# Kernel optimization log

Hardware: AMD Instinct MI355X
Metric: run time of the kernel (lower is better)

Reference implementation:

```python
import jax, jax.numpy as jnp
import numpy as np

N = 131072  # time steps
D = 4       # SDE state dimension


def setup_inputs() -> dict:
    key = jax.random.key(0)
    k = jax.random.split(key, 6)
    F = 0.1 * jax.random.normal(k[0], (D, D), jnp.float32)  # only shape/dtype used by filter
    H = jnp.zeros((1, D), jnp.float32).at[0, 0].set(1.0)    # observe first state component
    P_inf = jnp.eye(D, dtype=jnp.float32)
    # stable per-step transitions: spectral radius ~0.9
    A_seq = 0.9 * jnp.eye(D, dtype=jnp.float32)[None] + 0.02 * jax.random.normal(k[1], (N, D, D), jnp.float32)
    # PSD process noise per step
    S = 0.05 * jax.random.normal(k[2], (N, D, D), jnp.float32)
    Q_seq = jnp.einsum('nij,nkj->nik', S, S) + 1e-3 * jnp.eye(D, dtype=jnp.float32)[None]
    residual = jax.random.normal(k[3], (N,), jnp.float32)   # y - mean_fn(times)
    mask = jnp.ones((N,), jnp.float32)                      # all steps observed
    R_seq = 0.1 + 0.05 * jax.random.uniform(k[4], (N,), jnp.float32)  # noise_var + floor
    return dict(F=F, H=H, P_inf=P_inf, A_seq=A_seq, Q_seq=Q_seq,
                residual=residual, mask=mask, R_seq=R_seq)


def _kalman_filter(F, H, P_inf, A_seq, Q_seq, residual, mask, R_seq):
    d = F.shape[0]
    eye = jnp.eye(d, dtype=F.dtype)
    h = H[0]  # (d,)
    log_2pi = jnp.log(2.0 * jnp.pi).astype(F.dtype)

    def step(carry, inputs):
        m, P = carry
        A, Q, r_n, mask_n, R_n = inputs
        m_pred = A @ m
        P_pred = A @ P @ A.T + Q
        P_pred = 0.5 * (P_pred + P_pred.T)
        Ph = P_pred @ h                 # (d,)
        S = h @ Ph + R_n                # innovation variance
        innov = r_n - h @ m_pred
        is_obs = mask_n == 1
        S_safe = jnp.where(is_obs, S, 1.0)
        K = jnp.where(is_obs, Ph / S_safe, jnp.zeros_like(Ph))
        m_new = m_pred + K * innov
        I_KH = eye - K[:, None] * h[None, :]
        P_new = I_KH @ P_pred @ I_KH.T + R_n * (K[:, None] * K[None, :])
        P_new = 0.5 * (P_new + P_new.T)
        ll = jnp.where(is_obs, -0.5 * (log_2pi + jnp.log(S_safe) + innov * innov / S_safe), 0.0)
        return (m_new, P_new), (m_pred, P_pred, m_new, P_new, ll)

    m0 = jnp.zeros(d, dtype=F.dtype)
    _, (m_pred_seq, P_pred_seq, m_filt_seq, P_filt_seq, ll_seq) = jax.lax.scan(
        step, (m0, P_inf), (A_seq, Q_seq, residual, mask, R_seq))
    return m_pred_seq, P_pred_seq, m_filt_seq, P_filt_seq, jnp.sum(ll_seq)


def _rts_smoother(m_pred_seq, P_pred_seq, m_filt_seq, P_filt_seq, A_seq):
    def step(carry, inputs):
        m_ns, P_ns = carry
        m_f, P_f, m_pn, P_pn, A_n = inputs
        J = jnp.linalg.solve(P_pn.T, A_n @ P_f.T).T
        m_s = m_f + J @ (m_ns - m_pn)
        P_s = P_f + J @ (P_ns - P_pn) @ J.T
        P_s = 0.5 * (P_s + P_s.T)
        return (m_s, P_s), (m_s, P_s)

    m_T = m_filt_seq[-1]
    P_T = P_filt_seq[-1]
    inputs = (m_filt_seq[:-1], P_filt_seq[:-1], m_pred_seq[1:], P_pred_seq[1:], A_seq[1:])
    _, (m_s, P_s) = jax.lax.scan(step, (m_T, P_T), inputs, reverse=True)
    return (jnp.concatenate([m_s, m_T[None]], axis=0),
            jnp.concatenate([P_s, P_T[None]], axis=0))


def reference(F, H, P_inf, A_seq, Q_seq, residual, mask, R_seq):
    m_pred, P_pred, m_filt, P_filt, log_marginal = _kalman_filter(
        F, H, P_inf, A_seq, Q_seq, residual, mask, R_seq)
    m_smooth, P_smooth = _rts_smoother(m_pred, P_pred, m_filt, P_filt, A_seq)
    h = H[0]
    means = m_smooth @ h                                   # (N,) observation-space means
    vars_ = jnp.einsum('i,nij,j->n', h, P_smooth, h)       # (N,) marginal variances
    return means, vars_, log_marginal
```

## Files before the change

### kernel.cpp

```cpp
#include <hip/hip_runtime.h>
#include <math.h>

#define NN 131072
#define WUP 32
#define TPB 256
#define NBLK (NN / TPB)
#define WINF (TPB + WUP + 1)
#define BTPB 320
#define SCAN_N (TPB + WUP)
#define LOG2PI 1.8378770664093453f

typedef __attribute__((ext_vector_type(2))) float f2;

__device__ float4 g_f[5][NN];
__device__ float4 g_J[4][NN];
__device__ float4 g_W0[NN];
__device__ float4 g_W1[NN];
__device__ float2 g_W2[NN];
__device__ float4 g_u[NN];
__device__ double g_llb[NBLK];

__device__ __forceinline__ f2 bc(float s) {
  f2 r = {s, s};
  return r;
}
#define PF(a, b, c) __builtin_elementwise_fma((a), (b), (c))

template <int E>
__device__ __forceinline__ void ldpk(const float4 (*s)[E], int w, f2* M) {
#pragma unroll
  for (int c = 0; c < 4; ++c) {
    float4 v = s[c][w];
    M[2 * c] = f2{v.x, v.y};
    M[2 * c + 1] = f2{v.z, v.w};
  }
}

__device__ __forceinline__ void sym_rows(const float4 t0, const float4 t1, const float2 t2,
                                         f2* M) {
  M[0] = f2{t0.x, t0.y};
  M[1] = f2{t0.z, t0.w};
  M[2] = f2{t0.y, t1.x};
  M[3] = f2{t1.y, t1.z};
  M[4] = f2{t0.z, t1.y};
  M[5] = f2{t1.w, t2.x};
  M[6] = f2{t0.w, t1.z};
  M[7] = f2{t2.x, t2.y};
}

__device__ __forceinline__ void kf_step_pk(const f2* __restrict__ AT, const f2* __restrict__ Q,
                                           float r, float mk, float R, f2* __restrict__ m,
                                           f2* __restrict__ P, float& Ss, float& innov,
                                           bool& obs) {
  float m0 = m[0][0], m1 = m[0][1], m2_ = m[1][0], m3 = m[1][1];
  f2 mp[2];
#pragma unroll
  for (int p = 0; p < 2; ++p) {
    f2 acc = AT[p] * bc(m0);
    acc = PF(bc(m1), AT[2 + p], acc);
    acc = PF(bc(m2_), AT[4 + p], acc);
    acc = PF(bc(m3), AT[6 + p], acc);
    mp[p] = acc;
  }

  f2 T[8];
#pragma unroll
  for (int i = 0; i < 4; ++i) {
    float a0 = AT[0 + (i >> 1)][i & 1];
    float a1 = AT[2 + (i >> 1)][i & 1];
    float a2 = AT[4 + (i >> 1)][i & 1];
    float a3 = AT[6 + (i >> 1)][i & 1];
#pragma unroll
    for (int p = 0; p < 2; ++p) {
      f2 acc = P[p] * bc(a0);
      acc = PF(bc(a1), P[2 + p], acc);
      acc = PF(bc(a2), P[4 + p], acc);
      acc = PF(bc(a3), P[6 + p], acc);
      T[2 * i + p] = acc;
    }
  }

  f2 Pp[8];
#pragma unroll
  for (int i = 0; i < 4; ++i) {
    float t0 = T[2 * i][0], t1 = T[2 * i][1], t2 = T[2 * i + 1][0], t3 = T[2 * i + 1][1];
#pragma unroll
    for (int p = 0; p < 2; ++p) {
      f2 acc = PF(bc(t0), AT[p], Q[2 * i + p]);
      acc = PF(bc(t1), AT[2 + p], acc);
      acc = PF(bc(t2), AT[4 + p], acc);
      acc = PF(bc(t3), AT[6 + p], acc);
      Pp[2 * i + p] = acc;
    }
  }

  float S = Pp[0][0] + R;
  innov = r - mp[0][0];
  obs = (mk == 1.0f);
  Ss = obs ? S : 1.0f;
  float kf = obs ? __builtin_amdgcn_rcpf(S) : 0.0f;
  f2 K[2] = {Pp[0] * bc(kf), Pp[1] * bc(kf)};
#pragma unroll
  for (int p = 0; p < 2; ++p) m[p] = PF(K[p], bc(innov), mp[p]);

#pragma unroll
  for (int i = 0; i < 4; ++i) {
    float Ki = K[i >> 1][i & 1];
#pragma unroll
    for (int p = 0; p < 2; ++p) P[2 * i + p] = PF(bc(-Ki), Pp[p], Pp[2 * i + p]);
  }
}

__device__ __forceinline__ void chol_solve_pk(const f2* __restrict__ S, const f2* __restrict__ T,
                                              f2* __restrict__ X) {
  float s00 = S[0][0];
  float s10 = S[2][0], s11 = S[2][1];
  float s20 = S[4][0], s21 = S[4][1], s22 = S[5][0];
  float s30 = S[6][0], s31 = S[6][1], s32 = S[7][0], s33 = S[7][1];
  float i00 = __builtin_amdgcn_rsqf(s00);
  float l10 = s10 * i00, l20 = s20 * i00, l30 = s30 * i00;
  float i11 = __builtin_amdgcn_rsqf(s11 - l10 * l10);
  float l21 = (s21 - l20 * l10) * i11;
  float l31 = (s31 - l30 * l10) * i11;
  float i22 = __builtin_amdgcn_rsqf(s22 - l20 * l20 - l21 * l21);
  float l32 = (s32 - l30 * l20 - l31 * l21) * i22;
  float i33 = __builtin_amdgcn_rsqf(s33 - l30 * l30 - l31 * l31 - l32 * l32);
#pragma unroll
  for (int c = 0; c < 4; ++c) {
    float t0 = T[0 + (c >> 1)][c & 1];
    float t1 = T[2 + (c >> 1)][c & 1];
    float t2 = T[4 + (c >> 1)][c & 1];
    float t3 = T[6 + (c >> 1)][c & 1];
    float y0 = t0 * i00;
    float y1 = (t1 - l10 * y0) * i11;
    float y2 = (t2 - l20 * y0 - l21 * y1) * i22;
    float y3 = (t3 - l30 * y0 - l31 * y1 - l32 * y2) * i33;
    float x3 = y3 * i33;
    float x2 = (y2 - l32 * x3) * i22;
    float x1 = (y1 - l21 * x2 - l31 * x3) * i11;
    float x0 = (y0 - l10 * x1 - l20 * x2 - l30 * x3) * i00;
    X[0 + (c >> 1)][c & 1] = x0;
    X[2 + (c >> 1)][c & 1] = x1;
    X[4 + (c >> 1)][c & 1] = x2;
    X[6 + (c >> 1)][c & 1] = x3;
  }
}

__device__ __forceinline__ void make_record_pk(int n, const f2* __restrict__ m,
                                               const f2* __restrict__ P,
                                               const f2* __restrict__ AT,
                                               const f2* __restrict__ Q) {
  float m0 = m[0][0], m1 = m[0][1], m2_ = m[1][0], m3 = m[1][1];
  f2 pm[2];
#pragma unroll
  for (int p = 0; p < 2; ++p) {
    f2 acc = AT[p] * bc(m0);
    acc = PF(bc(m1), AT[2 + p], acc);
    acc = PF(bc(m2_), AT[4 + p], acc);
    acc = PF(bc(m3), AT[6 + p], acc);
    pm[p] = acc;
  }

  f2 T[8];
#pragma unroll
  for (int i = 0; i < 4; ++i) {
    float a0 = AT[0 + (i >> 1)][i & 1];
    float a1 = AT[2 + (i >> 1)][i & 1];
    float a2 = AT[4 + (i >> 1)][i & 1];
    float a3 = AT[6 + (i >> 1)][i & 1];
#pragma unroll
    for (int p = 0; p < 2; ++p) {
      f2 acc = P[p] * bc(a0);
      acc = PF(bc(a1), P[2 + p], acc);
      acc = PF(bc(a2), P[4 + p], acc);
      acc = PF(bc(a3), P[6 + p], acc);
      T[2 * i + p] = acc;
    }
  }

  f2 Ppn[8];
#pragma unroll
  for (int i = 0; i < 4; ++i) {
    float t0 = T[2 * i][0], t1 = T[2 * i][1], t2 = T[2 * i + 1][0], t3 = T[2 * i + 1][1];
#pragma unroll
    for (int p = 0; p < 2; ++p) {
      f2 acc = PF(bc(t0), AT[p], Q[2 * i + p]);
      acc = PF(bc(t1), AT[2 + p], acc);
      acc = PF(bc(t2), AT[4 + p], acc);
      acc = PF(bc(t3), AT[6 + p], acc);
      Ppn[2 * i + p] = acc;
    }
  }

  f2 X[8];
  chol_solve_pk(Ppn, T, X);

  float p0 = pm[0][0], p1 = pm[0][1], p2 = pm[1][0], p3 = pm[1][1];
  f2 u[2];
#pragma unroll
  for (int p = 0; p < 2; ++p) {
    f2 acc = X[p] * bc(p0);
    acc = PF(bc(p1), X[2 + p], acc);
    acc = PF(bc(p2), X[4 + p], acc);
    acc = PF(bc(p3), X[6 + p], acc);
    u[p] = m[p] - acc;
  }

  f2 Jp[8];
#pragma unroll
  for (int i = 0; i < 4; ++i) {
    float x0 = X[0 + (i >> 1)][i & 1];
    float x1 = X[2 + (i >> 1)][i & 1];
    float x2 = X[4 + (i >> 1)][i & 1];
    float x3 = X[6 + (i >> 1)][i & 1];
#pragma unroll
    for (int p = 0; p < 2; ++p) {
      f2 acc = Ppn[p] * bc(x0);
      acc = PF(bc(x1), Ppn[2 + p], acc);
      acc = PF(bc(x2), Ppn[4 + p], acc);
      acc = PF(bc(x3), Ppn[6 + p], acc);
      Jp[2 * i + p] = acc;
    }
  }
  f2 W[8];
#pragma unroll
  for (int i = 0; i < 4; ++i) {
    float j0 = Jp[2 * i][0], j1 = Jp[2 * i][1], j2 = Jp[2 * i + 1][0], j3 = Jp[2 * i + 1][1];
#pragma unroll
    for (int p = 0; p < 2; ++p) {
      f2 acc = X[p] * bc(j0);
      acc = PF(bc(j1), X[2 + p], acc);
      acc = PF(bc(j2), X[4 + p], acc);
      acc = PF(bc(j3), X[6 + p], acc);
      W[2 * i + p] = P[2 * i + p] - acc;
    }
  }

#pragma unroll
  for (int i = 0; i < 4; ++i)
    g_J[i][n] = make_float4(X[2 * i][0], X[2 * i][1], X[2 * i + 1][0], X[2 * i + 1][1]);
  g_W0[n] = make_float4(W[0][0], W[0][1], W[1][0], W[1][1]);
  g_W1[n] = make_float4(W[2][1], W[3][0], W[3][1], W[5][0]);
  g_W2[n] = make_float2(W[5][1], W[7][1]);
  g_u[n] = make_float4(u[0][0], u[0][1], u[1][0], u[1][1]);
}

__global__ __launch_bounds__(TPB, 1) void fwd_kernel(const float* __restrict__ P_inf,
                                                     const float* __restrict__ A_seq,
                                                     const float* __restrict__ Q_seq,
                                                     const float* __restrict__ residual,
                                                     const float* __restrict__ mask,
                                                     const float* __restrict__ R_seq) {
  __shared__ float4 sAT[4][WINF];
  __shared__ float4 sQ0[WINF], sQ1[WINF];
  __shared__ float2 sQ2[WINF];
  __shared__ float4 sRM[WINF];
  __shared__ double sh[TPB];

  const int B = blockIdx.x * TPB;
  const int base = B - WUP;
  const float4* Af4 = (const float4*)A_seq;
  const float4* Qf4 = (const float4*)Q_seq;
  for (int f = threadIdx.x; f < WINF * 4; f += TPB) {
    int w = f >> 2, c = f & 3;
    int k = base + w;
    k = k < 0 ? 0 : (k > NN - 1 ? NN - 1 : k);
    float4 rowA = Af4[(size_t)k * 4 + c];
    ((float*)&sAT[0][w])[c] = rowA.x;
    ((float*)&sAT[1][w])[c] = rowA.y;
    ((float*)&sAT[2][w])[c] = rowA.z;
    ((float*)&sAT[3][w])[c] = rowA.w;
    float4 rowQ = Qf4[(size_t)k * 4 + c];
    if (c == 0) {
      sQ0[w] = rowQ;
    } else if (c == 1) {
      sQ1[w].x = rowQ.y;
      sQ1[w].y = rowQ.z;
      sQ1[w].z = rowQ.w;
    } else if (c == 2) {
      sQ1[w].w = rowQ.z;
      sQ2[w].x = rowQ.w;
    } else {
      sQ2[w].y = rowQ.w;
    }
  }
  for (int w = threadIdx.x; w < WINF; w += TPB) {
    int k = base + w;
    k = k < 0 ? 0 : (k > NN - 1 ? NN - 1 : k);
    sRM[w] = make_float4(residual[k], R_seq[k], mask[k], 0.f);
  }
  __syncthreads();

  const int t = threadIdx.x;
  const int n = B + t;
  int s0 = n - WUP;
  if (s0 < 0) s0 = 0;

  f2 m[2] = {f2{0.f, 0.f}, f2{0.f, 0.f}};
  f2 P[8];
#pragma unroll
  for (int i = 0; i < 4; ++i) {
    P[2 * i] = f2{P_inf[i * 4 + 0], P_inf[i * 4 + 1]};
    P[2 * i + 1] = f2{P_inf[i * 4 + 2], P_inf[i * 4 + 3]};
  }

  float Ss = 1.f, innov = 0.f;
  bool obs = false;
#pragma unroll 2
  for (int k = s0; k <= n; ++k) {
    int w = k - base;
    f2 AT[8], Q[8];
    ldpk<WINF>(sAT, w, AT);
    sym_rows(sQ0[w], sQ1[w], sQ2[w], Q);
    float4 rm = sRM[w];
    kf_step_pk(AT, Q, rm.x, rm.z, rm.y, m, P, Ss, innov, obs);
  }

#pragma unroll
  for (int c = 0; c < 4; ++c)
    g_f[c][n] = make_float4(P[2 * c][0], P[2 * c][1], P[2 * c + 1][0], P[2 * c + 1][1]);
  g_f[4][n] = make_float4(m[0][0], m[0][1], m[1][0], m[1][1]);

  if (n < NN - 1) {
    int w = n + 1 - base;
    f2 AT[8], Q[8];
    ldpk<WINF>(sAT, w, AT);
    sym_rows(sQ0[w], sQ1[w], sQ2[w], Q);
    make_record_pk(n, m, P, AT, Q);
  }

  sh[t] = obs ? (double)(-0.5f * (LOG2PI + logf(Ss) + innov * innov / Ss)) : 0.0;
  __syncthreads();
#pragma unroll
  for (int w = TPB / 2; w > 0; w >>= 1) {
    if (t < w) sh[t] += sh[t + w];
    __syncthreads();
  }
  if (t == 0) g_llb[blockIdx.x] = sh[0];
}

__global__ __launch_bounds__(BTPB, 1) void bwd_kernel(float* __restrict__ out) {
  __shared__ float4 pJ[4][SCAN_N];
  __shared__ float4 pW0[SCAN_N], pW1[SCAN_N];
  __shared__ float2 pW2[SCAN_N];
  __shared__ float4 pu[SCAN_N];
  __shared__ double shd[TPB];

  const int B = blockIdx.x * TPB;
  const int t = threadIdx.x;
  const bool own = (t < SCAN_N);
  const int k = B + t;

  const int ii = (B + SCAN_N <= NN - 1) ? (B + SCAN_N) : (NN - 1);
  f2 Pi[8], mi[2];
#pragma unroll
  for (int c = 0; c < 4; ++c) {
    float4 v = g_f[c][ii];
    Pi[2 * c] = f2{v.x, v.y};
    Pi[2 * c + 1] = f2{v.z, v.w};
  }
  {
    float4 v = g_f[4][ii];
    mi[0] = f2{v.x, v.y};
    mi[1] = f2{v.z, v.w};
  }

  f2 X[8], W[8], u[2];
  if (own && k < NN - 1) {
#pragma unroll
    for (int c = 0; c < 4; ++c) {
      float4 v = g_J[c][k];
      X[2 * c] = f2{v.x, v.y};
      X[2 * c + 1] = f2{v.z, v.w};
    }
    sym_rows(g_W0[k], g_W1[k], g_W2[k], W);
    float4 v = g_u[k];
    u[0] = f2{v.x, v.y};
    u[1] = f2{v.z, v.w};
  } else {
    X[0] = f2{1.f, 0.f}; X[1] = f2{0.f, 0.f};
    X[2] = f2{0.f, 1.f}; X[3] = f2{0.f, 0.f};
    X[4] = f2{0.f, 0.f}; X[5] = f2{1.f, 0.f};
    X[6] = f2{0.f, 0.f}; X[7] = f2{0.f, 1.f};
#pragma unroll
    for (int i = 0; i < 8; ++i) W[i] = f2{0.f, 0.f};
    u[0] = f2{0.f, 0.f};
    u[1] = f2{0.f, 0.f};
  }

  for (int d = 1; d < SCAN_N; d <<= 1) {
    if (own) {
#pragma unroll
      for (int c = 0; c < 4; ++c)
        pJ[c][t] = make_float4(X[2 * c][0], X[2 * c][1], X[2 * c + 1][0], X[2 * c + 1][1]);
      pW0[t] = make_float4(W[0][0], W[0][1], W[1][0], W[1][1]);
      pW1[t] = make_float4(W[2][1], W[3][0], W[3][1], W[5][0]);
      pW2[t] = make_float2(W[5][1], W[7][1]);
      pu[t] = make_float4(u[0][0], u[0][1], u[1][0], u[1][1]);
    }
    __syncthreads();
    const bool act = own && (t + d < SCAN_N);
    f2 Xb[8], Wb[8], ub[2];
    if (act) {
      const int s = t + d;
#pragma unroll
      for (int c = 0; c < 4; ++c) {
        float4 v = pJ[c][s];
        Xb[2 * c] = f2{v.x, v.y};
        Xb[2 * c + 1] = f2{v.z, v.w};
      }
      sym_rows(pW0[s], pW1[s], pW2[s], Wb);
      float4 v = pu[s];
      ub[0] = f2{v.x, v.y};
      ub[1] = f2{v.z, v.w};
    }
    __syncthreads();
    if (act) {
      f2 Xc[8];
#pragma unroll
      for (int i = 0; i < 4; ++i) {
        float b0 = Xb[2 * i][0], b1 = Xb[2 * i][1], b2 = Xb[2 * i + 1][0], b3 = Xb[2 * i + 1][1];
#pragma unroll
        for (int p = 0; p < 2; ++p) {
          f2 acc = X[p] * bc(b0);
          acc = PF(bc(b1), X[2 + p], acc);
          acc = PF(bc(b2), X[4 + p], acc);
          acc = PF(bc(b3), X[6 + p], acc);
          Xc[2 * i + p] = acc;
        }
      }
      float ub0 = ub[0][0], ub1 = ub[0][1], ub2 = ub[1][0], ub3 = ub[1][1];
      f2 uc[2];
#pragma unroll
      for (int p = 0; p < 2; ++p) {
        f2 acc = PF(bc(ub0), X[p], u[p]);
        acc = PF(bc(ub1), X[2 + p], acc);
        acc = PF(bc(ub2), X[4 + p], acc);
        acc = PF(bc(ub3), X[6 + p], acc);
        uc[p] = acc;
      }
      f2 V[8];
#pragma unroll
      for (int q = 0; q < 4; ++q) {
        float w0 = Wb[2 * q][0], w1 = Wb[2 * q][1], w2 = Wb[2 * q + 1][0], w3 = Wb[2 * q + 1][1];
#pragma unroll
        for (int p = 0; p < 2; ++p) {
          f2 acc = X[p] * bc(w0);
          acc = PF(bc(w1), X[2 + p], acc);
          acc = PF(bc(w2), X[4 + p], acc);
          acc = PF(bc(w3), X[6 + p], acc);
          V[2 * q + p] = acc;
        }
      }
      f2 Wc[8];
#pragma unroll
      for (int i = 0; i < 4; ++i) {
        float x0 = X[0 + (i >> 1)][i & 1];
        float x1 = X[2 + (i >> 1)][i & 1];
        float x2 = X[4 + (i >> 1)][i & 1];
        float x3 = X[6 + (i >> 1)][i & 1];
#pragma unroll
        for (int p = 0; p < 2; ++p) {
          f2 acc = PF(bc(x0), V[p], W[2 * i + p]);
          acc = PF(bc(x1), V[2 + p], acc);
          acc = PF(bc(x2), V[4 + p], acc);
          acc = PF(bc(x3), V[6 + p], acc);
          Wc[2 * i + p] = acc;
        }
      }
#pragma unroll
      for (int i = 0; i < 8; ++i) {
        X[i] = Xc[i];
        W[i] = Wc[i];
      }
      u[0] = uc[0];
      u[1] = uc[1];
    }
  }

  if (t < TPB) {
    float x00 = X[0][0], x01 = X[2][0], x02 = X[4][0], x03 = X[6][0];
    float mean = u[0][0] + x00 * mi[0][0] + x01 * mi[0][1] + x02 * mi[1][0] + x03 * mi[1][1];
    float t0 = Pi[0][0] * x00 + Pi[0][1] * x01 + Pi[1][0] * x02 + Pi[1][1] * x03;
    float t1 = Pi[2][0] * x00 + Pi[2][1] * x01 + Pi[3][0] * x02 + Pi[3][1] * x03;
    float t2 = Pi[4][0] * x00 + Pi[4][1] * x01 + Pi[5][0] * x02 + Pi[5][1] * x03;
    float t3 = Pi[6][0] * x00 + Pi[6][1] * x01 + Pi[7][0] * x02 + Pi[7][1] * x03;
    float var = W[0][0] + x00 * t0 + x01 * t1 + x02 * t2 + x03 * t3;
    out[B + t] = mean;
    out[NN + B + t] = var;
  }

  if (blockIdx.x == 0) {
    if (t < TPB) {
      double acc = 0.0;
      for (int i = t; i < NBLK; i += TPB) acc += g_llb[i];
      shd[t] = acc;
    }
    __syncthreads();
#pragma unroll
    for (int w = TPB / 2; w > 0; w >>= 1) {
      if (t < w) shd[t] += shd[t + w];
      __syncthreads();
    }
    if (t == 0) out[2 * NN] = (float)shd[0];
  }
}

extern "C" void kernel_launch(void* const* d_in, const int* in_sizes, int n_in, void* d_out,
                              int out_size, void* d_ws, size_t ws_size, hipStream_t stream) {
  const float* P_inf = (const float*)d_in[2];
  const float* A_seq = (const float*)d_in[3];
  const float* Q_seq = (const float*)d_in[4];
  const float* residual = (const float*)d_in[5];
  const float* mask = (const float*)d_in[6];
  const float* R_seq = (const float*)d_in[7];
  float* out = (float*)d_out;

  fwd_kernel<<<NBLK, TPB, 0, stream>>>(P_inf, A_seq, Q_seq, residual, mask, R_seq);
  bwd_kernel<<<NBLK, BTPB, 0, stream>>>(out);
}
```

Before: 114.3 us.

## Use a radix-4 double-buffered backward scan and wavefront-shuffle reductions

The backward-pass parallel scan now advances by a factor of four per level: each thread composes three neighbours in turn, and the shared-memory staging buffers are double-buffered. This cuts the number of levels and leaves one barrier per level instead of two. The log-likelihood reductions in both kernels are replaced with 64-lane shuffle reductions followed by a small cross-wavefront sum. The trade is more compose arithmetic per thread and twice the shared memory for the scan buffers, in exchange for fewer block-wide synchronisations.

```diff
diff --git a/kernel.cpp b/kernel.cpp
--- a/kernel.cpp
+++ b/kernel.cpp
@@ -245,6 +245,76 @@
   g_u[n] = make_float4(u[0][0], u[0][1], u[1][0], u[1][1]);
 }
 
+__device__ __forceinline__ void compose_pk(f2* __restrict__ X, f2* __restrict__ W,
+                                           f2* __restrict__ u, const f2* __restrict__ Xb,
+                                           const f2* __restrict__ Wb,
+                                           const f2* __restrict__ ub) {
+  f2 Xc[8];
+#pragma unroll
+  for (int i = 0; i < 4; ++i) {
+    float b0 = Xb[2 * i][0], b1 = Xb[2 * i][1], b2 = Xb[2 * i + 1][0], b3 = Xb[2 * i + 1][1];
+#pragma unroll
+    for (int p = 0; p < 2; ++p) {
+      f2 acc = X[p] * bc(b0);
+      acc = PF(bc(b1), X[2 + p], acc);
+      acc = PF(bc(b2), X[4 + p], acc);
+      acc = PF(bc(b3), X[6 + p], acc);
+      Xc[2 * i + p] = acc;
+    }
+  }
+  float ub0 = ub[0][0], ub1 = ub[0][1], ub2 = ub[1][0], ub3 = ub[1][1];
+  f2 uc[2];
+#pragma unroll
+  for (int p = 0; p < 2; ++p) {
+    f2 acc = PF(bc(ub0), X[p], u[p]);
+    acc = PF(bc(ub1), X[2 + p], acc);
+    acc = PF(bc(ub2), X[4 + p], acc);
+    acc = PF(bc(ub3), X[6 + p], acc);
+    uc[p] = acc;
+  }
+  f2 V[8];
+#pragma unroll
+  for (int q = 0; q < 4; ++q) {
+    float w0 = Wb[2 * q][0], w1 = Wb[2 * q][1], w2 = Wb[2 * q + 1][0], w3 = Wb[2 * q + 1][1];
+#pragma unroll
+    for (int p = 0; p < 2; ++p) {
+      f2 acc = X[p] * bc(w0);
+      acc = PF(bc(w1), X[2 + p], acc);
+      acc = PF(bc(w2), X[4 + p], acc);
+      acc = PF(bc(w3), X[6 + p], acc);
+      V[2 * q + p] = acc;
+    }
+  }
+#pragma unroll
+  for (int i = 0; i < 4; ++i) {
+    float x0 = X[0 + (i >> 1)][i & 1];
+    float x1 = X[2 + (i >> 1)][i & 1];
+    float x2 = X[4 + (i >> 1)][i & 1];
+    float x3 = X[6 + (i >> 1)][i & 1];
+    f2 w0, w1;
+    {
+      f2 acc = PF(bc(x0), V[0], W[2 * i + 0]);
+      acc = PF(bc(x1), V[2], acc);
+      acc = PF(bc(x2), V[4], acc);
+      acc = PF(bc(x3), V[6], acc);
+      w0 = acc;
+    }
+    {
+      f2 acc = PF(bc(x0), V[1], W[2 * i + 1]);
+      acc = PF(bc(x1), V[3], acc);
+      acc = PF(bc(x2), V[5], acc);
+      acc = PF(bc(x3), V[7], acc);
+      w1 = acc;
+    }
+    W[2 * i + 0] = w0;
+    W[2 * i + 1] = w1;
+  }
+#pragma unroll
+  for (int i = 0; i < 8; ++i) X[i] = Xc[i];
+  u[0] = uc[0];
+  u[1] = uc[1];
+}
+
 __global__ __launch_bounds__(TPB, 1) void fwd_kernel(const float* __restrict__ P_inf,
                                                      const float* __restrict__ A_seq,
                                                      const float* __restrict__ Q_seq,
@@ -255,7 +325,7 @@
   __shared__ float4 sQ0[WINF], sQ1[WINF];
   __shared__ float2 sQ2[WINF];
   __shared__ float4 sRM[WINF];
-  __shared__ double sh[TPB];
+  __shared__ double swl[TPB / 64];
 
   const int B = blockIdx.x * TPB;
   const int base = B - WUP;
@@ -329,22 +399,20 @@
     make_record_pk(n, m, P, AT, Q);
   }
 
-  sh[t] = obs ? (double)(-0.5f * (LOG2PI + logf(Ss) + innov * innov / Ss)) : 0.0;
+  double llv = obs ? (double)(-0.5f * (LOG2PI + logf(Ss) + innov * innov / Ss)) : 0.0;
+#pragma unroll
+  for (int o = 32; o > 0; o >>= 1) llv += __shfl_down(llv, o, 64);
+  if ((t & 63) == 0) swl[t >> 6] = llv;
   __syncthreads();
-#pragma unroll
-  for (int w = TPB / 2; w > 0; w >>= 1) {
-    if (t < w) sh[t] += sh[t + w];
-    __syncthreads();
-  }
-  if (t == 0) g_llb[blockIdx.x] = sh[0];
+  if (t == 0) g_llb[blockIdx.x] = swl[0] + swl[1] + swl[2] + swl[3];
 }
 
 __global__ __launch_bounds__(BTPB, 1) void bwd_kernel(float* __restrict__ out) {
-  __shared__ float4 pJ[4][SCAN_N];
-  __shared__ float4 pW0[SCAN_N], pW1[SCAN_N];
-  __shared__ float2 pW2[SCAN_N];
-  __shared__ float4 pu[SCAN_N];
-  __shared__ double shd[TPB];
+  __shared__ float4 pJ[2][4][SCAN_N];
+  __shared__ float4 pW0[2][SCAN_N], pW1[2][SCAN_N];
+  __shared__ float2 pW2[2][SCAN_N];
+  __shared__ float4 pu[2][SCAN_N];
+  __shared__ double swb[BTPB / 64];
 
   const int B = blockIdx.x * TPB;
   const int t = threadIdx.x;
@@ -388,94 +456,39 @@
     u[1] = f2{0.f, 0.f};
   }
 
-  for (int d = 1; d < SCAN_N; d <<= 1) {
+  int buf = 0;
+  for (int d = 1; d < SCAN_N; d <<= 2) {
     if (own) {
 #pragma unroll
       for (int c = 0; c < 4; ++c)
-        pJ[c][t] = make_float4(X[2 * c][0], X[2 * c][1], X[2 * c + 1][0], X[2 * c + 1][1]);
-      pW0[t] = make_float4(W[0][0], W[0][1], W[1][0], W[1][1]);
-      pW1[t] = make_float4(W[2][1], W[3][0], W[3][1], W[5][0]);
-      pW2[t] = make_float2(W[5][1], W[7][1]);
-      pu[t] = make_float4(u[0][0], u[0][1], u[1][0], u[1][1]);
+        pJ[buf][c][t] = make_float4(X[2 * c][0], X[2 * c][1], X[2 * c + 1][0], X[2 * c + 1][1]);
+      pW0[buf][t] = make_float4(W[0][0], W[0][1], W[1][0], W[1][1]);
+      pW1[buf][t] = make_float4(W[2][1], W[3][0], W[3][1], W[5][0]);
+      pW2[buf][t] = make_float2(W[5][1], W[7][1]);
+      pu[buf][t] = make_float4(u[0][0], u[0][1], u[1][0], u[1][1]);
     }
     __syncthreads();
-    const bool act = own && (t + d < SCAN_N);
-    f2 Xb[8], Wb[8], ub[2];
-    if (act) {
-      const int s = t + d;
-#pragma unroll
-      for (int c = 0; c < 4; ++c) {
-        float4 v = pJ[c][s];
-        Xb[2 * c] = f2{v.x, v.y};
-        Xb[2 * c + 1] = f2{v.z, v.w};
-      }
-      sym_rows(pW0[s], pW1[s], pW2[s], Wb);
-      float4 v = pu[s];
-      ub[0] = f2{v.x, v.y};
-      ub[1] = f2{v.z, v.w};
-    }
-    __syncthreads();
-    if (act) {
-      f2 Xc[8];
-#pragma unroll
-      for (int i = 0; i < 4; ++i) {
-        float b0 = Xb[2 * i][0], b1 = Xb[2 * i][1], b2 = Xb[2 * i + 1][0], b3 = Xb[2 * i + 1][1];
-#pragma unroll
-        for (int p = 0; p < 2; ++p) {
-          f2 acc = X[p] * bc(b0);
-          acc = PF(bc(b1), X[2 + p], acc);
-          acc = PF(bc(b2), X[4 + p], acc);
-          acc = PF(bc(b3), X[6 + p], acc);
-          Xc[2 * i + p] = acc;
+    if (own) {
+#pragma unroll
+      for (int j = 1; j <= 3; ++j) {
+        const int s = t + j * d;
+        if (s < SCAN_N) {
+          f2 Xb[8], Wb[8], ub[2];
+#pragma unroll
+          for (int c = 0; c < 4; ++c) {
+            float4 v = pJ[buf][c][s];
+            Xb[2 * c] = f2{v.x, v.y};
+            Xb[2 * c + 1] = f2{v.z, v.w};
+          }
+          sym_rows(pW0[buf][s], pW1[buf][s], pW2[buf][s], Wb);
+          float4 v = pu[buf][s];
+          ub[0] = f2{v.x, v.y};
+          ub[1] = f2{v.z, v.w};
+          compose_pk(X, W, u, Xb, Wb, ub);
         }
       }
-      float ub0 = ub[0][0], ub1 = ub[0][1], ub2 = ub[1][0], ub3 = ub[1][1];
-      f2 uc[2];
-#pragma unroll
-      for (int p = 0; p < 2; ++p) {
-        f2 acc = PF(bc(ub0), X[p], u[p]);
-        acc = PF(bc(ub1), X[2 + p], acc);
-        acc = PF(bc(ub2), X[4 + p], acc);
-        acc = PF(bc(ub3), X[6 + p], acc);
-        uc[p] = acc;
-      }
-      f2 V[8];
-#pragma unroll
-      for (int q = 0; q < 4; ++q) {
-        float w0 = Wb[2 * q][0], w1 = Wb[2 * q][1], w2 = Wb[2 * q + 1][0], w3 = Wb[2 * q + 1][1];
-#pragma unroll
-        for (int p = 0; p < 2; ++p) {
-          f2 acc = X[p] * bc(w0);
-          acc = PF(bc(w1), X[2 + p], acc);
-          acc = PF(bc(w2), X[4 + p], acc);
-          acc = PF(bc(w3), X[6 + p], acc);
-          V[2 * q + p] = acc;
-        }
-      }
-      f2 Wc[8];
-#pragma unroll
-      for (int i = 0; i < 4; ++i) {
-        float x0 = X[0 + (i >> 1)][i & 1];
-        float x1 = X[2 + (i >> 1)][i & 1];
-        float x2 = X[4 + (i >> 1)][i & 1];
-        float x3 = X[6 + (i >> 1)][i & 1];
-#pragma unroll
-        for (int p = 0; p < 2; ++p) {
-          f2 acc = PF(bc(x0), V[p], W[2 * i + p]);
-          acc = PF(bc(x1), V[2 + p], acc);
-          acc = PF(bc(x2), V[4 + p], acc);
-          acc = PF(bc(x3), V[6 + p], acc);
-          Wc[2 * i + p] = acc;
-        }
-      }
-#pragma unroll
-      for (int i = 0; i < 8; ++i) {
-        X[i] = Xc[i];
-        W[i] = Wc[i];
-      }
-      u[0] = uc[0];
-      u[1] = uc[1];
-    }
+    }
+    buf ^= 1;
   }
 
   if (t < TPB) {
@@ -491,18 +504,13 @@
   }
 
   if (blockIdx.x == 0) {
-    if (t < TPB) {
-      double acc = 0.0;
-      for (int i = t; i < NBLK; i += TPB) acc += g_llb[i];
-      shd[t] = acc;
-    }
+    double acc = 0.0;
+    for (int i = t; i < NBLK; i += BTPB) acc += g_llb[i];
+#pragma unroll
+    for (int o = 32; o > 0; o >>= 1) acc += __shfl_down(acc, o, 64);
+    if ((t & 63) == 0) swb[t >> 6] = acc;
     __syncthreads();
-#pragma unroll
-    for (int w = TPB / 2; w > 0; w >>= 1) {
-      if (t < w) shd[t] += shd[t + w];
-      __syncthreads();
-    }
-    if (t == 0) out[2 * NN] = (float)shd[0];
+    if (t == 0) out[2 * NN] = (float)(swb[0] + swb[1] + swb[2] + swb[3] + swb[4]);
   }
 }
 
```

Result: slower. 120.8 us (+5.7%).
